# Performance work log

Hardware: AMD Instinct MI355X
Metric: run time of the kernel (lower is better)

The kernel has to match this reference:

```python
import jax, jax.numpy as jnp
import numpy as np

B, S, D, H = 4, 1024, 1024, 16
HD = D // H  # head_dim = 64


def setup_inputs() -> dict:
    key = jax.random.key(0)
    k1, k2, k3, k4 = jax.random.split(key, 4)
    scale = 1.0 / np.sqrt(D)
    return {
        "x": jax.random.normal(k1, (B, S, D), dtype=jnp.float32),
        "w_qkv": jax.random.normal(k2, (3 * D, D), dtype=jnp.float32) * scale,
        "w_out": jax.random.normal(k3, (D, D), dtype=jnp.float32) * scale,
        "b_out": jax.random.normal(k4, (D,), dtype=jnp.float32) * scale,
    }


def reference(x, w_qkv, w_out, b_out):
    b, s, d_model = x.shape
    # qkv linear (no bias): (b, s, 3*D); torch Linear computes x @ W.T
    qkv = x @ w_qkv.T
    # Rearrange 'b s (qkv h hd) -> qkv b h s hd'
    qkv = qkv.reshape(b, s, 3, H, HD).transpose(2, 0, 3, 1, 4)
    q, k, v = qkv[0], qkv[1], qkv[2]
    scale = HD ** -0.5
    att = jax.nn.softmax(jnp.einsum('bhxd,bhyd->bhxy', q, k) * scale, axis=-1)
    out = jnp.einsum('bhxy,bhyd->bhxd', att, v)  # (b, h, s, hd)
    out = out.transpose(0, 2, 1, 3).reshape(b, s, d_model)  # 'b h s hd -> b s (h hd)'
    return out @ w_out.T + b_out
```

## Files before the change

### kernel.cpp

```cpp
#include <hip/hip_runtime.h>
#include <hip/hip_bf16.h>
#include <stdint.h>

typedef unsigned short u16;
typedef __bf16 bf16x8 __attribute__((ext_vector_type(8)));
typedef u16 u16x8 __attribute__((ext_vector_type(8)));
typedef u16 u16x4 __attribute__((ext_vector_type(4)));
typedef float f32x4 __attribute__((ext_vector_type(4)));

#define MFMA_16x16x32(a, b, c) __builtin_amdgcn_mfma_f32_16x16x32_bf16((a), (b), (c), 0, 0, 0)

#if __has_builtin(__builtin_amdgcn_exp2f)
#define EXP2F(x) __builtin_amdgcn_exp2f(x)
#else
#define EXP2F(x) exp2f(x)
#endif

#define QSCALE_F 0.18033688011112042f

__device__ __forceinline__ u16 f2b(float f) {
  __bf16 h = (__bf16)f;
  return __builtin_bit_cast(u16, h);
}

__device__ __forceinline__ void store_c(u16* C, size_t idx, float v) { C[idx] = f2b(v); }
__device__ __forceinline__ void store_c(float* C, size_t idx, float v) { C[idx] = v; }

__device__ __forceinline__ void gload16(const void* g, void* l) {
  __builtin_amdgcn_global_load_lds(
      (const __attribute__((address_space(1))) unsigned int*)(uintptr_t)(g),
      (__attribute__((address_space(3))) unsigned int*)(uintptr_t)(l),
      16, 0, 0);
}

__device__ __forceinline__ bf16x8 load_frag(const u16* Ls, int off) {
  return *(const bf16x8*)(Ls + off);
}
__device__ __forceinline__ bf16x8 load_frag(const float* Ls, int off) {
  f32x4 lo = *(const f32x4*)(Ls + off);
  f32x4 hi = *(const f32x4*)(Ls + off + 4);
  bf16x8 r;
#pragma unroll
  for (int e = 0; e < 4; e++) {
    r[e] = (__bf16)lo[e];
    r[e + 4] = (__bf16)hi[e];
  }
  return r;
}

template <typename T, int ROWS>
__device__ __forceinline__ void stage_tile(const T* __restrict__ G, int ldg, int tr, int k0,
                                           T* Ls, int wave, int lane) {
  constexpr int EPL = 16 / sizeof(T);
  constexpr int PCE = 64 * EPL;
  constexpr int CALLS = (ROWS * 32) / (4 * PCE);
#pragma unroll
  for (int ci = 0; ci < CALLS; ci++) {
    const int base = (wave * CALLS + ci) * PCE;
    const int idx0 = base + lane * EPL;
    const int r = idx0 >> 5;
    const int c = idx0 & 31;
    gload16(G + (size_t)(tr + r) * ldg + k0 + c, Ls + base);
  }
}

template <typename TA, typename TB, typename TC, bool BIAS, bool QSC, int TM>
__global__ __launch_bounds__(256) void gemm_bt(const TA* __restrict__ A,
                                               const TB* __restrict__ B,
                                               const float* __restrict__ bias,
                                               TC* __restrict__ C,
                                               int M, int N, int K) {
  constexpr int MI = TM >> 5;
  __shared__ TA As[2][TM * 32];
  __shared__ TB Bs[2][128 * 32];
  const int tid = threadIdx.x;
  const int lane = tid & 63;
  const int wave = tid >> 6;
  const int l15 = lane & 15;
  const int g = lane >> 4;
  const int g8 = g * 8;
  const int cpx = (int)gridDim.x >> 3;
  const int bid = ((int)blockIdx.x & 7) * cpx + ((int)blockIdx.x >> 3);
  const int tiles_n = N >> 7;
  const int tm = (bid / tiles_n) * TM;
  const int tn = (bid % tiles_n) << 7;
  const int wm = (wave >> 1) * (TM >> 1);
  const int wn = (wave & 1) << 6;

  f32x4 acc[MI][4] = {};

  const int nt = K >> 5;
  stage_tile<TA, TM>(A, K, tm, 0, As[0], wave, lane);
  stage_tile<TB, 128>(B, K, tn, 0, Bs[0], wave, lane);
  __syncthreads();

  for (int t = 0; t < nt; t++) {
    const int cur = t & 1;
    if (t + 1 < nt) {
      stage_tile<TA, TM>(A, K, tm, (t + 1) << 5, As[cur ^ 1], wave, lane);
      stage_tile<TB, 128>(B, K, tn, (t + 1) << 5, Bs[cur ^ 1], wave, lane);
    }
    bf16x8 af[MI], bfr[4];
#pragma unroll
    for (int i = 0; i < MI; i++) af[i] = load_frag(As[cur], (wm + i * 16 + l15) * 32 + g8);
#pragma unroll
    for (int i = 0; i < 4; i++) bfr[i] = load_frag(Bs[cur], (wn + i * 16 + l15) * 32 + g8);
#pragma unroll
    for (int mi = 0; mi < MI; mi++)
#pragma unroll
      for (int nj = 0; nj < 4; nj++)
        acc[mi][nj] = MFMA_16x16x32(af[mi], bfr[nj], acc[mi][nj]);
    __syncthreads();
  }

  float bv[4], cs[4];
#pragma unroll
  for (int nj = 0; nj < 4; nj++) {
    const int col = tn + wn + nj * 16 + l15;
    bv[nj] = BIAS ? bias[col] : 0.0f;
    cs[nj] = (QSC && col < 1024) ? QSCALE_F : 1.0f;
  }

#pragma unroll
  for (int mi = 0; mi < MI; mi++) {
#pragma unroll
    for (int nj = 0; nj < 4; nj++) {
      const int row = tm + wm + mi * 16 + g * 4;
      const int col = tn + wn + nj * 16 + l15;
#pragma unroll
      for (int r = 0; r < 4; r++)
        store_c(C, (size_t)(row + r) * N + col, (acc[mi][nj][r] + bv[nj]) * cs[nj]);
    }
  }
}

__global__ __launch_bounds__(256) void cvt_bf16(const float* __restrict__ in,
                                                u16* __restrict__ out, int n8) {
  const int i = blockIdx.x * 256 + threadIdx.x;
  if (i >= n8) return;
  const f32x4* p = (const f32x4*)in + (size_t)i * 2;
  f32x4 a = p[0], b = p[1];
  u16x8 r;
#pragma unroll
  for (int e = 0; e < 4; e++) {
    r[e] = f2b(a[e]);
    r[e + 4] = f2b(b[e]);
  }
  *((u16x8*)out + i) = r;
}

__device__ __forceinline__ int swz64(int row) { return ((row >> 3) ^ row) & 7; }

__global__ __launch_bounds__(256) void attn(const u16* __restrict__ qkv,
                                            u16* __restrict__ attout) {
  __shared__ u16 Ks[2][64 * 64];
  __shared__ u16 Vs[2][64 * 64];
  __shared__ u16 Pl[4][32 * 64];
  const int tid = threadIdx.x;
  const int lane = tid & 63;
  const int w = tid >> 6;
  const int l15 = lane & 15;
  const int g = lane >> 4;
  const int g8 = g * 8;

  const int bid = blockIdx.x;
  const int xs = bid & 7;
  const int j = bid >> 3;
  const int bh = xs * 8 + (j >> 3);
  const int qt = j & 7;
  const int b = bh >> 4;
  const int h = bh & 15;
  const size_t rowbase = (size_t)b * 1024;
  const int qcol = h * 64;

  const int qr0 = qt * 128 + w * 32;
  bf16x8 qf[2][2];
#pragma unroll
  for (int mi = 0; mi < 2; mi++)
#pragma unroll
    for (int ks = 0; ks < 2; ks++)
      qf[mi][ks] =
          *(const bf16x8*)&qkv[(rowbase + qr0 + mi * 16 + l15) * 3072 + qcol + ks * 32 + g8];

  f32x4 o[2][4] = {};
  float l_r[2][4] = {};

  const int vh3 = tid & 7;
  const int vhc = vh3 << 3;
  const int vkey0 = tid >> 3;
  bf16x8 vreg[2];

  auto loadV = [&](int kt) {
    vreg[0] = *(const bf16x8*)&qkv[(rowbase + kt * 64 + vkey0) * 3072 + 2048 + qcol + vhc];
    vreg[1] = *(const bf16x8*)&qkv[(rowbase + kt * 64 + vkey0 + 32) * 3072 + 2048 + qcol + vhc];
  };
  auto writeV = [&](int buf) {
#pragma unroll
    for (int it = 0; it < 2; it++) {
      const int key = vkey0 + it * 32;
      const int pos = ((key & 15) << 2) | (key >> 4);
      const u16* vu = (const u16*)&vreg[it];
#pragma unroll
      for (int e = 0; e < 8; e++) {
        const int sl = (vh3 ^ e) & 7;
        Vs[buf][(vhc + e) * 64 + (pos ^ (sl << 3))] = vu[e];
      }
    }
  };
  auto stageK = [&](int buf, int kt) {
#pragma unroll
    for (int ci = 0; ci < 2; ci++) {
      const int ch = ci * 64 + lane;
      const int row = w * 16 + (ch >> 3);
      const int cc = (ch & 7) ^ swz64(row);
      gload16(&qkv[(rowbase + kt * 64 + row) * 3072 + 1024 + qcol + cc * 8],
              &Ks[buf][w * 1024 + ci * 512]);
    }
  };

  stageK(0, 0);
  loadV(0);
  writeV(0);
  __syncthreads();

  for (int kt = 0; kt < 16; kt++) {
    const int cur = kt & 1;
    if (kt < 15) {
      stageK(cur ^ 1, kt + 1);
      loadV(kt + 1);
    }

    f32x4 s[2][4] = {};
#pragma unroll
    for (int nj = 0; nj < 4; nj++) {
      const int key = nj * 16 + l15;
      const int sk = swz64(key) << 3;
#pragma unroll
      for (int ks = 0; ks < 2; ks++) {
        const bf16x8 kfr = *(const bf16x8*)&Ks[cur][key * 64 + ((ks * 32 + g8) ^ sk)];
#pragma unroll
        for (int mi = 0; mi < 2; mi++)
          s[mi][nj] = MFMA_16x16x32(qf[mi][ks], kfr, s[mi][nj]);
      }
    }

#pragma unroll
    for (int mi = 0; mi < 2; mi++)
#pragma unroll
      for (int r = 0; r < 4; r++) {
        const float p0 = EXP2F(s[mi][0][r]);
        const float p1 = EXP2F(s[mi][1][r]);
        const float p2 = EXP2F(s[mi][2][r]);
        const float p3 = EXP2F(s[mi][3][r]);
        l_r[mi][r] += (p0 + p1) + (p2 + p3);
        const int row = mi * 16 + g * 4 + r;
        const int sq = swz64(row) << 3;
        u16x4 pk;
        pk[0] = f2b(p0);
        pk[1] = f2b(p1);
        pk[2] = f2b(p2);
        pk[3] = f2b(p3);
        *(u16x4*)&Pl[w][row * 64 + ((l15 << 2) ^ sq)] = pk;
      }

    bf16x8 pf[2][2];
#pragma unroll
    for (int mi = 0; mi < 2; mi++) {
      const int pr = mi * 16 + l15;
      const int sp = swz64(pr) << 3;
#pragma unroll
      for (int ks = 0; ks < 2; ks++)
        pf[mi][ks] = *(const bf16x8*)&Pl[w][pr * 64 + ((ks * 32 + g8) ^ sp)];
    }
#pragma unroll
    for (int nj = 0; nj < 4; nj++) {
      const int hd = nj * 16 + l15;
      const int sv = swz64(hd) << 3;
#pragma unroll
      for (int ks = 0; ks < 2; ks++) {
        const bf16x8 vf = *(const bf16x8*)&Vs[cur][hd * 64 + ((ks * 32 + g8) ^ sv)];
#pragma unroll
        for (int mi = 0; mi < 2; mi++)
          o[mi][nj] = MFMA_16x16x32(pf[mi][ks], vf, o[mi][nj]);
      }
    }

    if (kt < 15) writeV(cur ^ 1);
    __syncthreads();
  }

#pragma unroll
  for (int mi = 0; mi < 2; mi++)
#pragma unroll
    for (int r = 0; r < 4; r++) {
      float v = l_r[mi][r];
#pragma unroll
      for (int d = 1; d < 16; d <<= 1) v += __shfl_xor(v, d, 64);
      l_r[mi][r] = v;
    }

#pragma unroll
  for (int mi = 0; mi < 2; mi++) {
    float inv[4];
#pragma unroll
    for (int r = 0; r < 4; r++) inv[r] = 1.0f / l_r[mi][r];
#pragma unroll
    for (int nj = 0; nj < 4; nj++)
#pragma unroll
      for (int r = 0; r < 4; r++)
        attout[(rowbase + qr0 + mi * 16 + g * 4 + r) * 1024 + qcol + nj * 16 + l15] =
            f2b(o[mi][nj][r] * inv[r]);
  }
}

extern "C" void kernel_launch(void* const* d_in, const int* in_sizes, int n_in,
                              void* d_out, int out_size, void* d_ws, size_t ws_size,
                              hipStream_t stream) {
  const float* x = (const float*)d_in[0];
  const float* w_qkv = (const float*)d_in[1];
  const float* w_out = (const float*)d_in[2];
  const float* b_out = (const float*)d_in[3];
  float* out = (float*)d_out;

  u16* qkv = (u16*)d_ws;
  u16* attout = qkv + 12582912;
  const size_t needA = 39845888ull;

  if (ws_size >= needA) {
    u16* xb = attout;
    u16* wqb = attout + 4194304;
    u16* wob = wqb;
    cvt_bf16<<<dim3(2048), dim3(256), 0, stream>>>(x, xb, 524288);
    cvt_bf16<<<dim3(1536), dim3(256), 0, stream>>>(w_qkv, wqb, 393216);
    gemm_bt<u16, u16, u16, false, true, 128><<<dim3(32 * 24), dim3(256), 0, stream>>>(
        xb, wqb, nullptr, qkv, 4096, 3072, 1024);
    cvt_bf16<<<dim3(512), dim3(256), 0, stream>>>(w_out, wob, 131072);
    attn<<<dim3(512), dim3(256), 0, stream>>>(qkv, attout);
    gemm_bt<u16, u16, float, true, false, 64><<<dim3(64 * 8), dim3(256), 0, stream>>>(
        attout, wob, b_out, out, 4096, 1024, 1024);
  } else {
    gemm_bt<float, float, u16, false, true, 128><<<dim3(32 * 24), dim3(256), 0, stream>>>(
        x, w_qkv, nullptr, qkv, 4096, 3072, 1024);
    attn<<<dim3(512), dim3(256), 0, stream>>>(qkv, attout);
    gemm_bt<u16, float, float, true, false, 64><<<dim3(64 * 8), dim3(256), 0, stream>>>(
        attout, w_out, b_out, out, 4096, 1024, 1024);
  }
}
```

Baseline: 102.0 us.

## Swizzle GEMM LDS tiles and load attention K fragments directly from global

The GEMM stage_tile and fragment loads now use an XOR column swizzle on the LDS tiles, both for bf16 and for fp32 inputs, to reduce bank conflicts on fragment reads. In the attention kernel, the double-buffered K shared-memory staging is removed, and each wave loads its K fragments straight from global memory (L2) into registers for each key tile. This frees LDS and avoids the K-staging traffic, but it adds uncovered global-load latency inside the loop and redundant K reads across the four waves.

```diff
diff --git a/kernel.cpp b/kernel.cpp
--- a/kernel.cpp
+++ b/kernel.cpp
@@ -33,20 +33,6 @@
       16, 0, 0);
 }
 
-__device__ __forceinline__ bf16x8 load_frag(const u16* Ls, int off) {
-  return *(const bf16x8*)(Ls + off);
-}
-__device__ __forceinline__ bf16x8 load_frag(const float* Ls, int off) {
-  f32x4 lo = *(const f32x4*)(Ls + off);
-  f32x4 hi = *(const f32x4*)(Ls + off + 4);
-  bf16x8 r;
-#pragma unroll
-  for (int e = 0; e < 4; e++) {
-    r[e] = (__bf16)lo[e];
-    r[e + 4] = (__bf16)hi[e];
-  }
-  return r;
-}
 
 template <typename T, int ROWS>
 __device__ __forceinline__ void stage_tile(const T* __restrict__ G, int ldg, int tr, int k0,
@@ -60,8 +46,32 @@
     const int idx0 = base + lane * EPL;
     const int r = idx0 >> 5;
     const int c = idx0 & 31;
-    gload16(G + (size_t)(tr + r) * ldg + k0 + c, Ls + base);
-  }
+    int csw;
+    if constexpr (sizeof(T) == 2)
+      csw = ((c >> 3) ^ (r & 3)) << 3;
+    else
+      csw = ((c >> 2) ^ (r & 7)) << 2;
+    gload16(G + (size_t)(tr + r) * ldg + k0 + csw, Ls + base);
+  }
+}
+
+__device__ __forceinline__ bf16x8 load_frag_sw(const u16* Ls, int row, int g8) {
+  const int c = ((g8 >> 3) ^ (row & 3)) << 3;
+  return *(const bf16x8*)(Ls + row * 32 + c);
+}
+__device__ __forceinline__ bf16x8 load_frag_sw(const float* Ls, int row, int g8) {
+  const int g2 = g8 >> 2;
+  const int c0 = (g2 ^ (row & 7)) << 2;
+  const int c1 = ((g2 + 1) ^ (row & 7)) << 2;
+  f32x4 lo = *(const f32x4*)(Ls + row * 32 + c0);
+  f32x4 hi = *(const f32x4*)(Ls + row * 32 + c1);
+  bf16x8 r;
+#pragma unroll
+  for (int e = 0; e < 4; e++) {
+    r[e] = (__bf16)lo[e];
+    r[e + 4] = (__bf16)hi[e];
+  }
+  return r;
 }
 
 template <typename TA, typename TB, typename TC, bool BIAS, bool QSC, int TM>
@@ -102,9 +112,9 @@
     }
     bf16x8 af[MI], bfr[4];
 #pragma unroll
-    for (int i = 0; i < MI; i++) af[i] = load_frag(As[cur], (wm + i * 16 + l15) * 32 + g8);
-#pragma unroll
-    for (int i = 0; i < 4; i++) bfr[i] = load_frag(Bs[cur], (wn + i * 16 + l15) * 32 + g8);
+    for (int i = 0; i < MI; i++) af[i] = load_frag_sw(As[cur], wm + i * 16 + l15, g8);
+#pragma unroll
+    for (int i = 0; i < 4; i++) bfr[i] = load_frag_sw(Bs[cur], wn + i * 16 + l15, g8);
 #pragma unroll
     for (int mi = 0; mi < MI; mi++)
 #pragma unroll
@@ -153,7 +163,6 @@
 
 __global__ __launch_bounds__(256) void attn(const u16* __restrict__ qkv,
                                             u16* __restrict__ attout) {
-  __shared__ u16 Ks[2][64 * 64];
   __shared__ u16 Vs[2][64 * 64];
   __shared__ u16 Pl[4][32 * 64];
   const int tid = threadIdx.x;
@@ -207,42 +216,33 @@
       }
     }
   };
-  auto stageK = [&](int buf, int kt) {
-#pragma unroll
-    for (int ci = 0; ci < 2; ci++) {
-      const int ch = ci * 64 + lane;
-      const int row = w * 16 + (ch >> 3);
-      const int cc = (ch & 7) ^ swz64(row);
-      gload16(&qkv[(rowbase + kt * 64 + row) * 3072 + 1024 + qcol + cc * 8],
-              &Ks[buf][w * 1024 + ci * 512]);
-    }
-  };
-
-  stageK(0, 0);
+
   loadV(0);
   writeV(0);
   __syncthreads();
 
   for (int kt = 0; kt < 16; kt++) {
     const int cur = kt & 1;
-    if (kt < 15) {
-      stageK(cur ^ 1, kt + 1);
-      loadV(kt + 1);
-    }
-
-    f32x4 s[2][4] = {};
+    if (kt < 15) loadV(kt + 1);
+
+    const u16* kbase = &qkv[(rowbase + kt * 64) * 3072 + 1024 + qcol];
+    bf16x8 kf[4][2];
 #pragma unroll
     for (int nj = 0; nj < 4; nj++) {
       const int key = nj * 16 + l15;
-      const int sk = swz64(key) << 3;
-#pragma unroll
-      for (int ks = 0; ks < 2; ks++) {
-        const bf16x8 kfr = *(const bf16x8*)&Ks[cur][key * 64 + ((ks * 32 + g8) ^ sk)];
+#pragma unroll
+      for (int ks = 0; ks < 2; ks++)
+        kf[nj][ks] = *(const bf16x8*)&kbase[(size_t)key * 3072 + ks * 32 + g8];
+    }
+
+    f32x4 s[2][4] = {};
+#pragma unroll
+    for (int nj = 0; nj < 4; nj++)
+#pragma unroll
+      for (int ks = 0; ks < 2; ks++)
 #pragma unroll
         for (int mi = 0; mi < 2; mi++)
-          s[mi][nj] = MFMA_16x16x32(qf[mi][ks], kfr, s[mi][nj]);
-      }
-    }
+          s[mi][nj] = MFMA_16x16x32(qf[mi][ks], kf[nj][ks], s[mi][nj]);
 
 #pragma unroll
     for (int mi = 0; mi < 2; mi++)
```

Result: slower. 110.9 us (+8.7%).
